# Kernel tuning notes

Hardware: AMD Instinct MI355X
Metric: run time of the kernel (lower is better)

## Reference

```python
import jax, jax.numpy as jnp
import numpy as np

NUM_HEADS = 4
GN_GROUPS = 32
EPS = 1e-5


def setup_inputs() -> dict:
    key = jax.random.key(0)
    ks = jax.random.split(key, 6)
    B, C, H, W = 4, 256, 64, 64
    return {
        "x": jax.random.normal(ks[0], (B, C, H, W), dtype=jnp.float32),
        "gn_w": jnp.ones((C,), dtype=jnp.float32),
        "gn_b": jnp.zeros((C,), dtype=jnp.float32),
        "qkv_w": jax.random.normal(ks[1], (3 * C, C), dtype=jnp.float32) * 0.05,
        "qkv_b": jax.random.normal(ks[2], (3 * C,), dtype=jnp.float32) * 0.02,
        "proj_w": jax.random.normal(ks[3], (C, C), dtype=jnp.float32) * 0.05,
        "proj_b": jax.random.normal(ks[4], (C,), dtype=jnp.float32) * 0.02,
    }


def reference(x, gn_w, gn_b, qkv_w, qkv_b, proj_w, proj_b):
    b, c, h, w = x.shape
    L = h * w
    xf = x.reshape(b, c, L)

    # GroupNorm32: normalize over (channels_per_group, length) in float32
    xg = xf.reshape(b, GN_GROUPS, (c // GN_GROUPS) * L).astype(jnp.float32)
    mean = xg.mean(axis=-1, keepdims=True)
    var = xg.var(axis=-1, keepdims=True)
    xn = ((xg - mean) * jax.lax.rsqrt(var + EPS)).reshape(b, c, L).astype(x.dtype)
    xn = xn * gn_w[:, None] + gn_b[:, None]

    # 1x1 Conv1d == channel matmul: [3C, C] @ [b, C, L]
    qkv = jnp.einsum('oc,bcl->bol', qkv_w, xn) + qkv_b[:, None]

    # QKVAttentionLegacy
    ch = c // NUM_HEADS
    qkv_h = qkv.reshape(b * NUM_HEADS, 3 * ch, L)
    q, k, v = qkv_h[:, :ch], qkv_h[:, ch:2 * ch], qkv_h[:, 2 * ch:]
    scale = 1.0 / np.sqrt(np.sqrt(ch)).astype(np.float32)
    weight = jnp.einsum('bct,bcs->bts', q * scale, k * scale)  # [b*H, L, L]
    weight = jax.nn.softmax(weight.astype(jnp.float32), axis=-1).astype(qkv.dtype)
    a = jnp.einsum('bts,bcs->bct', weight, v).reshape(b, c, L)

    h_out = jnp.einsum('oc,bcl->bol', proj_w, a) + proj_b[:, None]
    return (xf + h_out).reshape(b, c, h, w)
```

## Files before the change

### kernel.cpp

```cpp
#include <hip/hip_runtime.h>
#include <math.h>

#define L 4096
#define C 256

typedef __attribute__((ext_vector_type(8))) short bf16x8;
typedef __attribute__((ext_vector_type(4))) short s16x4;
typedef __attribute__((ext_vector_type(4))) float f32x4;
typedef __attribute__((ext_vector_type(2))) unsigned int u32x2;
typedef __attribute__((ext_vector_type(4))) unsigned int u32x4;

#define MFMA16(a, b, c) __builtin_amdgcn_mfma_f32_16x16x32_bf16(a, b, c, 0, 0, 0)

static __device__ __forceinline__ short f2bf(float f) {
  union { float f; unsigned u; } x{f};
  unsigned r = (x.u + 0x7fffu + ((x.u >> 16) & 1u)) >> 16;
  return (short)r;
}
static __device__ __forceinline__ unsigned pack2(float a, float b) {
  return (unsigned)(unsigned short)f2bf(a) | ((unsigned)(unsigned short)f2bf(b) << 16);
}
static __device__ __forceinline__ unsigned ppack(float a, float b) {
  union { float f; unsigned u; } xa{a}, xb{b};
  return __builtin_amdgcn_perm(xb.u, xa.u, 0x07060302u);
}
static __device__ __forceinline__ void gload_lds16(const void* g, void* l) {
  __builtin_amdgcn_global_load_lds(
      (const __attribute__((address_space(1))) unsigned int*)g,
      (__attribute__((address_space(3))) unsigned int*)l, 16, 0, 0);
}

__global__ __launch_bounds__(256) void prep(const float* __restrict__ x,
    float* __restrict__ gnp, const float* __restrict__ wa,
    const float* __restrict__ wb, short* __restrict__ da,
    short* __restrict__ db) {
  int blk = blockIdx.x;
  int tid = threadIdx.x;
  if (blk < 512) {
    int bg = blk >> 2, q = blk & 3;
    const f32x4* xp = (const f32x4*)(x + (size_t)bg * 32768 + (size_t)q * 8192);
    float s = 0.f, ss = 0.f;
    #pragma unroll
    for (int i = 0; i < 8; ++i) {
      f32x4 v = xp[i * 256 + tid];
      s  += v[0] + v[1] + v[2] + v[3];
      ss += v[0]*v[0] + v[1]*v[1] + v[2]*v[2] + v[3]*v[3];
    }
    __shared__ float rs[256], rss[256];
    rs[tid] = s; rss[tid] = ss;
    __syncthreads();
    for (int off = 128; off > 0; off >>= 1) {
      if (tid < off) { rs[tid] += rs[tid + off]; rss[tid] += rss[tid + off]; }
      __syncthreads();
    }
    if (tid == 0) {
      gnp[(size_t)blk * 2]     = rs[0];
      gnp[(size_t)blk * 2 + 1] = rss[0];
    }
  } else {
    int i = (blk - 512) * 256 + tid;
    if (i < 768 * C) da[i] = f2bf(wa[i]);
    else db[i - 768 * C] = f2bf(wb[i - 768 * C]);
  }
}

__global__ __launch_bounds__(256) void gn_apply(const float* __restrict__ x,
    const float* __restrict__ gw, const float* __restrict__ gb,
    const float* __restrict__ gnp, short* __restrict__ xnT) {
  int bg = blockIdx.y;
  int b = bg >> 5, g = bg & 31;
  int tid = threadIdx.x;
  const float* xg = x + (size_t)bg * 32768;

  float s  = gnp[(size_t)(bg*4)*2]   + gnp[(size_t)(bg*4+1)*2] +
             gnp[(size_t)(bg*4+2)*2] + gnp[(size_t)(bg*4+3)*2];
  float ss = gnp[(size_t)(bg*4)*2+1]   + gnp[(size_t)(bg*4+1)*2+1] +
             gnp[(size_t)(bg*4+2)*2+1] + gnp[(size_t)(bg*4+3)*2+1];
  float mean = s * (1.f / 32768.f);
  float var  = ss * (1.f / 32768.f) - mean * mean;
  float rstd = rsqrtf(var + 1e-5f);

  float scl[8], sft[8];
  #pragma unroll
  for (int c = 0; c < 8; ++c) {
    float wv = gw[g * 8 + c], bv = gb[g * 8 + c];
    scl[c] = rstd * wv;
    sft[c] = bv - mean * rstd * wv;
  }

  short* outb = xnT + (size_t)b * L * C + g * 8;
  int lb = blockIdx.x * 1024 + tid * 4;
  f32x4 v[8];
  #pragma unroll
  for (int c = 0; c < 8; ++c)
    v[c] = *(const f32x4*)(xg + (size_t)c * L + lb);
  #pragma unroll
  for (int j = 0; j < 4; ++j) {
    u32x4 ov;
    #pragma unroll
    for (int cp = 0; cp < 4; ++cp)
      ov[cp] = pack2(v[2*cp][j]   * scl[2*cp]   + sft[2*cp],
                     v[2*cp+1][j] * scl[2*cp+1] + sft[2*cp+1]);
    *(u32x4*)(outb + (size_t)(lb + j) * C) = ov;
  }
}

__global__ __launch_bounds__(256) void qkv_mfma(const short* __restrict__ wq,
    const float* __restrict__ bias, const short* __restrict__ xnT,
    short* __restrict__ qT, short* __restrict__ kT, short* __restrict__ vB) {
  int tid = threadIdx.x;
  int wid = tid >> 6, lane = tid & 63, g = lane >> 4, lr = lane & 15;
  int oy = blockIdx.y;
  int o0 = oy * 64;
  int b  = blockIdx.z;
  int head = oy / 3, kind = oy % 3;
  int bh = b * 4 + head;
  int lw = blockIdx.x * 128 + wid * 32;
  const short* xb = xnT + (size_t)b * L * C;

  f32x4 acc[4][2];
  #pragma unroll
  for (int m = 0; m < 4; ++m)
    #pragma unroll
    for (int nt = 0; nt < 2; ++nt) acc[m][nt] = (f32x4)0.f;

  #pragma unroll 2
  for (int k0 = 0; k0 < C; k0 += 32) {
    bf16x8 af[4], bfr[2];
    #pragma unroll
    for (int m = 0; m < 4; ++m)
      af[m] = *(const bf16x8*)(wq + (size_t)(o0 + m * 16 + lr) * C + k0 + g * 8);
    #pragma unroll
    for (int nt = 0; nt < 2; ++nt)
      bfr[nt] = *(const bf16x8*)(xb + (size_t)(lw + nt * 16 + lr) * C + k0 + g * 8);
    #pragma unroll
    for (int m = 0; m < 4; ++m)
      #pragma unroll
      for (int nt = 0; nt < 2; ++nt)
        acc[m][nt] = MFMA16(af[m], bfr[nt], acc[m][nt]);
  }

  float sc = (kind == 0) ? 0.51014930f : (kind == 1) ? 0.35355339f : 1.0f;
  if (kind == 2) {
    #pragma unroll
    for (int m = 0; m < 4; ++m)
      #pragma unroll
      for (int nt = 0; nt < 2; ++nt)
        #pragma unroll
        for (int r = 0; r < 4; ++r) {
          int o = m * 16 + g * 4 + r;
          vB[((size_t)bh * 64 + o) * L + lw + nt * 16 + lr] =
              f2bf(acc[m][nt][r] + bias[o0 + o]);
        }
  } else {
    short* dst = (kind == 0 ? qT : kT);
    #pragma unroll
    for (int m = 0; m < 4; ++m)
      #pragma unroll
      for (int nt = 0; nt < 2; ++nt) {
        s16x4 pk;
        #pragma unroll
        for (int r = 0; r < 4; ++r)
          pk[r] = f2bf((acc[m][nt][r] + bias[o0 + m * 16 + g * 4 + r]) * sc);
        *(s16x4*)(dst + ((size_t)bh * L + lw + nt * 16 + lr) * 64 + m * 16 + g * 4) = pk;
      }
  }
}

__global__ __launch_bounds__(512) void attn_mfma(
    const short* __restrict__ qT, const short* __restrict__ kT,
    const short* __restrict__ vB, short* __restrict__ amatT) {
  int orig = blockIdx.x;
  int bid = (orig & 7) * 64 + (orig >> 3);
  int bh = bid >> 5, qb = bid & 31;
  int b = bh >> 2, h = bh & 3;
  int tid = threadIdx.x;
  int wid = tid >> 6, lane = tid & 63;
  int g = lane >> 4, lr = lane & 15;
  int tw = qb * 128 + wid * 16;
  int lx7 = lr & 7;
  int pswA = ((lr & 3) << 4) | ((lr >> 2) << 2);

  const short* qTh = qT + (size_t)bh * L * 64;
  const short* kTh = kT + (size_t)bh * L * 64;
  const short* vh  = vB + (size_t)bh * 64 * L;

  __shared__ short Kt[4][64 * 64];
  __shared__ short Vt[4][64 * 64];
  __shared__ short plds[8][16][64];

  bf16x8 qf[2];
  #pragma unroll
  for (int ks = 0; ks < 2; ++ks)
    qf[ks] = *(const bf16x8*)(qTh + (size_t)(tw + lr) * 64 + ks * 32 + g * 8);

  bf16x8 ones;
  #pragma unroll
  for (int i = 0; i < 8; ++i) ones[i] = (short)0x3F80;

  f32x4 acc[4], acc_l;
  #pragma unroll
  for (int cm = 0; cm < 4; ++cm) acc[cm] = (f32x4)0.f;
  acc_l = (f32x4)0.f;

  size_t koff, voff;
  int ldsc;
  {
    int r = tid >> 3, c16 = tid & 7;
    int cs = c16 ^ (r & 7);
    koff = (size_t)r * 64 + cs * 8;
    voff = (size_t)r * L + cs * 8;
    ldsc = wid * 512;
  }

  gload_lds16(kTh + koff, &Kt[0][ldsc]);
  gload_lds16(vh + voff, &Vt[0][ldsc]);
  gload_lds16(kTh + koff + (size_t)64 * 64, &Kt[1][ldsc]);
  gload_lds16(vh + voff + 64, &Vt[1][ldsc]);

  int sl = 0;
  #pragma unroll 1
  for (int s = 0; s < 32; ++s) {
    if (s < 31) {
      int nb = sl ^ 2;
      size_t t0 = (size_t)(2 * s + 2) * 64, t1 = (size_t)(2 * s + 3) * 64;
      gload_lds16(kTh + koff + t0 * 64, &Kt[nb][ldsc]);
      gload_lds16(vh + voff + t0, &Vt[nb][ldsc]);
      gload_lds16(kTh + koff + t1 * 64, &Kt[nb + 1][ldsc]);
      gload_lds16(vh + voff + t1, &Vt[nb + 1][ldsc]);
      asm volatile("s_waitcnt vmcnt(4)" ::: "memory");
    } else {
      asm volatile("s_waitcnt vmcnt(0)" ::: "memory");
    }
    __builtin_amdgcn_sched_barrier(0);
    __builtin_amdgcn_s_barrier();

    const short* Ka = &Kt[sl][0];     const short* Va = &Vt[sl][0];
    const short* Kb = &Kt[sl + 1][0]; const short* Vb = &Vt[sl + 1][0];

    f32x4 st0[4], st1[4];
    __builtin_amdgcn_s_setprio(1);
    #pragma unroll
    for (int sm = 0; sm < 4; ++sm) {
      int row = sm * 16 + lr;
      bf16x8 kf0 = *(const bf16x8*)&Ka[row * 64 + (g ^ lx7) * 8];
      bf16x8 kf1 = *(const bf16x8*)&Ka[row * 64 + ((4 + g) ^ lx7) * 8];
      f32x4 cc = (f32x4)0.f;
      cc = MFMA16(kf0, qf[0], cc);
      cc = MFMA16(kf1, qf[1], cc);
      st0[sm] = cc;
    }
    __builtin_amdgcn_s_setprio(0);
    #pragma unroll
    for (int sm = 0; sm < 4; ++sm) {
      int row = sm * 16 + lr;
      bf16x8 kf0 = *(const bf16x8*)&Kb[row * 64 + (g ^ lx7) * 8];
      bf16x8 kf1 = *(const bf16x8*)&Kb[row * 64 + ((4 + g) ^ lx7) * 8];
      f32x4 cc = (f32x4)0.f;
      cc = MFMA16(kf0, qf[0], cc);
      cc = MFMA16(kf1, qf[1], cc);
      st1[sm] = cc;
      u32x2 w;
      w[0] = ppack(__builtin_amdgcn_exp2f(st0[sm][0]),
                   __builtin_amdgcn_exp2f(st0[sm][1]));
      w[1] = ppack(__builtin_amdgcn_exp2f(st0[sm][2]),
                   __builtin_amdgcn_exp2f(st0[sm][3]));
      *(u32x2*)&plds[wid][lr][(sm * 16 + g * 4) ^ pswA] = w;
    }
    bf16x8 pf0[2];
    #pragma unroll
    for (int ks = 0; ks < 2; ++ks) {
      s16x4 pa = *(const s16x4*)&plds[wid][lr][(ks * 32 + g * 8) ^ pswA];
      s16x4 pb = *(const s16x4*)&plds[wid][lr][(ks * 32 + g * 8 + 4) ^ pswA];
      pf0[ks] = __builtin_shufflevector(pa, pb, 0, 1, 2, 3, 4, 5, 6, 7);
    }
    acc_l = MFMA16(ones, pf0[0], acc_l);
    acc_l = MFMA16(ones, pf0[1], acc_l);
    #pragma unroll
    for (int cm = 0; cm < 4; ++cm) {
      int row = cm * 16 + lr;
      bf16x8 vf0 = *(const bf16x8*)&Va[row * 64 + (g ^ lx7) * 8];
      bf16x8 vf1 = *(const bf16x8*)&Va[row * 64 + ((4 + g) ^ lx7) * 8];
      acc[cm] = MFMA16(vf0, pf0[0], acc[cm]);
      acc[cm] = MFMA16(vf1, pf0[1], acc[cm]);
      u32x2 w;
      w[0] = ppack(__builtin_amdgcn_exp2f(st1[cm][0]),
                   __builtin_amdgcn_exp2f(st1[cm][1]));
      w[1] = ppack(__builtin_amdgcn_exp2f(st1[cm][2]),
                   __builtin_amdgcn_exp2f(st1[cm][3]));
      *(u32x2*)&plds[wid][lr][(cm * 16 + g * 4) ^ pswA] = w;
    }
    bf16x8 pf1[2];
    #pragma unroll
    for (int ks = 0; ks < 2; ++ks) {
      s16x4 pa = *(const s16x4*)&plds[wid][lr][(ks * 32 + g * 8) ^ pswA];
      s16x4 pb = *(const s16x4*)&plds[wid][lr][(ks * 32 + g * 8 + 4) ^ pswA];
      pf1[ks] = __builtin_shufflevector(pa, pb, 0, 1, 2, 3, 4, 5, 6, 7);
    }
    __builtin_amdgcn_s_setprio(1);
    acc_l = MFMA16(ones, pf1[0], acc_l);
    acc_l = MFMA16(ones, pf1[1], acc_l);
    #pragma unroll
    for (int cm = 0; cm < 4; ++cm) {
      int row = cm * 16 + lr;
      bf16x8 vf0 = *(const bf16x8*)&Vb[row * 64 + (g ^ lx7) * 8];
      bf16x8 vf1 = *(const bf16x8*)&Vb[row * 64 + ((4 + g) ^ lx7) * 8];
      acc[cm] = MFMA16(vf0, pf1[0], acc[cm]);
      acc[cm] = MFMA16(vf1, pf1[1], acc[cm]);
    }
    __builtin_amdgcn_s_setprio(0);
    __builtin_amdgcn_s_barrier();
    sl ^= 2;
  }

  float inv = 1.f / acc_l[0];
  #pragma unroll
  for (int cm = 0; cm < 4; ++cm) {
    s16x4 pk;
    #pragma unroll
    for (int r = 0; r < 4; ++r) pk[r] = f2bf(acc[cm][r] * inv);
    *(s16x4*)(amatT + ((size_t)b * L + tw + lr) * C + h * 64 + cm * 16 + g * 4) = pk;
  }
}

__global__ __launch_bounds__(256) void proj_mfma(const short* __restrict__ pw,
    const float* __restrict__ bias, const short* __restrict__ amatT,
    const float* __restrict__ xres, float* __restrict__ out) {
  int tid = threadIdx.x;
  int wid = tid >> 6, lane = tid & 63, g = lane >> 4, lr = lane & 15;
  int o0 = blockIdx.y * 64;
  int b  = blockIdx.z;
  int lw = blockIdx.x * 128 + wid * 32;
  const short* ab = amatT + (size_t)b * L * C;

  f32x4 acc[4][2];
  #pragma unroll
  for (int m = 0; m < 4; ++m)
    #pragma unroll
    for (int nt = 0; nt < 2; ++nt) acc[m][nt] = (f32x4)0.f;

  #pragma unroll 2
  for (int k0 = 0; k0 < C; k0 += 32) {
    bf16x8 af[4], bfr[2];
    #pragma unroll
    for (int m = 0; m < 4; ++m)
      af[m] = *(const bf16x8*)(pw + (size_t)(o0 + m * 16 + lr) * C + k0 + g * 8);
    #pragma unroll
    for (int nt = 0; nt < 2; ++nt)
      bfr[nt] = *(const bf16x8*)(ab + (size_t)(lw + nt * 16 + lr) * C + k0 + g * 8);
    #pragma unroll
    for (int m = 0; m < 4; ++m)
      #pragma unroll
      for (int nt = 0; nt < 2; ++nt)
        acc[m][nt] = MFMA16(af[m], bfr[nt], acc[m][nt]);
  }

  #pragma unroll
  for (int m = 0; m < 4; ++m)
    #pragma unroll
    for (int nt = 0; nt < 2; ++nt)
      #pragma unroll
      for (int r = 0; r < 4; ++r) {
        int o = o0 + m * 16 + g * 4 + r;
        size_t idx = ((size_t)b * C + o) * L + lw + nt * 16 + lr;
        out[idx] = acc[m][nt][r] + bias[o] + xres[idx];
      }
}

extern "C" void kernel_launch(void* const* d_in, const int* in_sizes, int n_in,
                              void* d_out, int out_size, void* d_ws, size_t ws_size,
                              hipStream_t stream) {
  const float* x      = (const float*)d_in[0];
  const float* gn_w   = (const float*)d_in[1];
  const float* gn_b   = (const float*)d_in[2];
  const float* qkv_w  = (const float*)d_in[3];
  const float* qkv_b  = (const float*)d_in[4];
  const float* proj_w = (const float*)d_in[5];
  const float* proj_b = (const float*)d_in[6];
  float* out = (float*)d_out;

  short* xnT   = (short*)d_ws;
  short* qT    = xnT   + (size_t)4 * L * C;
  short* kT    = qT    + (size_t)16 * L * 64;
  short* vB    = kT    + (size_t)16 * L * 64;
  short* amatT = vB    + (size_t)16 * L * 64;
  short* wqbf  = amatT + (size_t)4 * L * C;
  short* pwbf  = wqbf  + (size_t)768 * C;
  float* gnp   = (float*)(pwbf + (size_t)C * C);

  prep<<<1536, 256, 0, stream>>>(x, gnp, qkv_w, proj_w, wqbf, pwbf);
  gn_apply<<<dim3(4, 128), 256, 0, stream>>>(x, gn_w, gn_b, gnp, xnT);
  qkv_mfma<<<dim3(32, 12, 4), 256, 0, stream>>>(wqbf, qkv_b, xnT, qT, kT, vB);
  attn_mfma<<<512, 512, 0, stream>>>(qT, kT, vB, amatT);
  proj_mfma<<<dim3(32, 4, 4), 256, 0, stream>>>(pwbf, proj_b, amatT, x, out);
}
```

Measured before the change: 152.1 us.

## Process two 16-row query tiles per wave in attention to reuse K/V fragments

Each wave in the attention kernel now handles 32 query rows, as two 16-row tiles, instead of 16. The block therefore covers 256 queries and the grid halves from 512 to 256 blocks. Each K/V fragment read from LDS and each staged K/V tile is reused across twice as many MFMAs, cutting LDS and global traffic per unit of work. The cost is roughly double the accumulator and score registers, a larger P scratch buffer in LDS, and only 256 blocks on a 256-CU part, which lowers occupancy and may hurt latency hiding.

```diff
diff --git a/kernel.cpp b/kernel.cpp
--- a/kernel.cpp
+++ b/kernel.cpp
@@ -171,13 +171,13 @@
     const short* __restrict__ qT, const short* __restrict__ kT,
     const short* __restrict__ vB, short* __restrict__ amatT) {
   int orig = blockIdx.x;
-  int bid = (orig & 7) * 64 + (orig >> 3);
-  int bh = bid >> 5, qb = bid & 31;
+  int bid = (orig & 7) * 32 + (orig >> 3);
+  int bh = bid >> 4, qb = bid & 15;
   int b = bh >> 2, h = bh & 3;
   int tid = threadIdx.x;
   int wid = tid >> 6, lane = tid & 63;
   int g = lane >> 4, lr = lane & 15;
-  int tw = qb * 128 + wid * 16;
+  int tw = qb * 256 + wid * 32;
   int lx7 = lr & 7;
   int pswA = ((lr & 3) << 4) | ((lr >> 2) << 2);
 
@@ -187,21 +187,26 @@
 
   __shared__ short Kt[4][64 * 64];
   __shared__ short Vt[4][64 * 64];
-  __shared__ short plds[8][16][64];
-
-  bf16x8 qf[2];
-  #pragma unroll
-  for (int ks = 0; ks < 2; ++ks)
-    qf[ks] = *(const bf16x8*)(qTh + (size_t)(tw + lr) * 64 + ks * 32 + g * 8);
+  __shared__ short plds[8][32][64];
+
+  bf16x8 qf[2][2];
+  #pragma unroll
+  for (int nt = 0; nt < 2; ++nt)
+    #pragma unroll
+    for (int ks = 0; ks < 2; ++ks)
+      qf[nt][ks] = *(const bf16x8*)(qTh + (size_t)(tw + nt * 16 + lr) * 64 +
+                                    ks * 32 + g * 8);
 
   bf16x8 ones;
   #pragma unroll
   for (int i = 0; i < 8; ++i) ones[i] = (short)0x3F80;
 
-  f32x4 acc[4], acc_l;
-  #pragma unroll
-  for (int cm = 0; cm < 4; ++cm) acc[cm] = (f32x4)0.f;
-  acc_l = (f32x4)0.f;
+  f32x4 acc[4][2], acc_l[2];
+  #pragma unroll
+  for (int cm = 0; cm < 4; ++cm)
+    #pragma unroll
+    for (int nt = 0; nt < 2; ++nt) acc[cm][nt] = (f32x4)0.f;
+  acc_l[0] = (f32x4)0.f; acc_l[1] = (f32x4)0.f;
 
   size_t koff, voff;
   int ldsc;
@@ -238,17 +243,20 @@
     const short* Ka = &Kt[sl][0];     const short* Va = &Vt[sl][0];
     const short* Kb = &Kt[sl + 1][0]; const short* Vb = &Vt[sl + 1][0];
 
-    f32x4 st0[4], st1[4];
+    f32x4 st0[4][2], st1[4][2];
     __builtin_amdgcn_s_setprio(1);
     #pragma unroll
     for (int sm = 0; sm < 4; ++sm) {
       int row = sm * 16 + lr;
       bf16x8 kf0 = *(const bf16x8*)&Ka[row * 64 + (g ^ lx7) * 8];
       bf16x8 kf1 = *(const bf16x8*)&Ka[row * 64 + ((4 + g) ^ lx7) * 8];
-      f32x4 cc = (f32x4)0.f;
-      cc = MFMA16(kf0, qf[0], cc);
-      cc = MFMA16(kf1, qf[1], cc);
-      st0[sm] = cc;
+      #pragma unroll
+      for (int nt = 0; nt < 2; ++nt) {
+        f32x4 cc = (f32x4)0.f;
+        cc = MFMA16(kf0, qf[nt][0], cc);
+        cc = MFMA16(kf1, qf[nt][1], cc);
+        st0[sm][nt] = cc;
+      }
     }
     __builtin_amdgcn_s_setprio(0);
     #pragma unroll
@@ -256,70 +264,93 @@
       int row = sm * 16 + lr;
       bf16x8 kf0 = *(const bf16x8*)&Kb[row * 64 + (g ^ lx7) * 8];
       bf16x8 kf1 = *(const bf16x8*)&Kb[row * 64 + ((4 + g) ^ lx7) * 8];
-      f32x4 cc = (f32x4)0.f;
-      cc = MFMA16(kf0, qf[0], cc);
-      cc = MFMA16(kf1, qf[1], cc);
-      st1[sm] = cc;
-      u32x2 w;
-      w[0] = ppack(__builtin_amdgcn_exp2f(st0[sm][0]),
-                   __builtin_amdgcn_exp2f(st0[sm][1]));
-      w[1] = ppack(__builtin_amdgcn_exp2f(st0[sm][2]),
-                   __builtin_amdgcn_exp2f(st0[sm][3]));
-      *(u32x2*)&plds[wid][lr][(sm * 16 + g * 4) ^ pswA] = w;
-    }
-    bf16x8 pf0[2];
-    #pragma unroll
-    for (int ks = 0; ks < 2; ++ks) {
-      s16x4 pa = *(const s16x4*)&plds[wid][lr][(ks * 32 + g * 8) ^ pswA];
-      s16x4 pb = *(const s16x4*)&plds[wid][lr][(ks * 32 + g * 8 + 4) ^ pswA];
-      pf0[ks] = __builtin_shufflevector(pa, pb, 0, 1, 2, 3, 4, 5, 6, 7);
-    }
-    acc_l = MFMA16(ones, pf0[0], acc_l);
-    acc_l = MFMA16(ones, pf0[1], acc_l);
+      #pragma unroll
+      for (int nt = 0; nt < 2; ++nt) {
+        f32x4 cc = (f32x4)0.f;
+        cc = MFMA16(kf0, qf[nt][0], cc);
+        cc = MFMA16(kf1, qf[nt][1], cc);
+        st1[sm][nt] = cc;
+        u32x2 w;
+        w[0] = ppack(__builtin_amdgcn_exp2f(st0[sm][nt][0]),
+                     __builtin_amdgcn_exp2f(st0[sm][nt][1]));
+        w[1] = ppack(__builtin_amdgcn_exp2f(st0[sm][nt][2]),
+                     __builtin_amdgcn_exp2f(st0[sm][nt][3]));
+        *(u32x2*)&plds[wid][nt * 16 + lr][(sm * 16 + g * 4) ^ pswA] = w;
+      }
+    }
+    bf16x8 pf0[2][2];
+    #pragma unroll
+    for (int nt = 0; nt < 2; ++nt)
+      #pragma unroll
+      for (int ks = 0; ks < 2; ++ks) {
+        s16x4 pa = *(const s16x4*)&plds[wid][nt * 16 + lr][(ks * 32 + g * 8) ^ pswA];
+        s16x4 pb = *(const s16x4*)&plds[wid][nt * 16 + lr][(ks * 32 + g * 8 + 4) ^ pswA];
+        pf0[nt][ks] = __builtin_shufflevector(pa, pb, 0, 1, 2, 3, 4, 5, 6, 7);
+      }
+    #pragma unroll
+    for (int nt = 0; nt < 2; ++nt) {
+      acc_l[nt] = MFMA16(ones, pf0[nt][0], acc_l[nt]);
+      acc_l[nt] = MFMA16(ones, pf0[nt][1], acc_l[nt]);
+    }
     #pragma unroll
     for (int cm = 0; cm < 4; ++cm) {
       int row = cm * 16 + lr;
       bf16x8 vf0 = *(const bf16x8*)&Va[row * 64 + (g ^ lx7) * 8];
       bf16x8 vf1 = *(const bf16x8*)&Va[row * 64 + ((4 + g) ^ lx7) * 8];
-      acc[cm] = MFMA16(vf0, pf0[0], acc[cm]);
-      acc[cm] = MFMA16(vf1, pf0[1], acc[cm]);
-      u32x2 w;
-      w[0] = ppack(__builtin_amdgcn_exp2f(st1[cm][0]),
-                   __builtin_amdgcn_exp2f(st1[cm][1]));
-      w[1] = ppack(__builtin_amdgcn_exp2f(st1[cm][2]),
-                   __builtin_amdgcn_exp2f(st1[cm][3]));
-      *(u32x2*)&plds[wid][lr][(cm * 16 + g * 4) ^ pswA] = w;
-    }
-    bf16x8 pf1[2];
-    #pragma unroll
-    for (int ks = 0; ks < 2; ++ks) {
-      s16x4 pa = *(const s16x4*)&plds[wid][lr][(ks * 32 + g * 8) ^ pswA];
-      s16x4 pb = *(const s16x4*)&plds[wid][lr][(ks * 32 + g * 8 + 4) ^ pswA];
-      pf1[ks] = __builtin_shufflevector(pa, pb, 0, 1, 2, 3, 4, 5, 6, 7);
-    }
+      #pragma unroll
+      for (int nt = 0; nt < 2; ++nt) {
+        acc[cm][nt] = MFMA16(vf0, pf0[nt][0], acc[cm][nt]);
+        acc[cm][nt] = MFMA16(vf1, pf0[nt][1], acc[cm][nt]);
+        u32x2 w;
+        w[0] = ppack(__builtin_amdgcn_exp2f(st1[cm][nt][0]),
+                     __builtin_amdgcn_exp2f(st1[cm][nt][1]));
+        w[1] = ppack(__builtin_amdgcn_exp2f(st1[cm][nt][2]),
+                     __builtin_amdgcn_exp2f(st1[cm][nt][3]));
+        *(u32x2*)&plds[wid][nt * 16 + lr][(cm * 16 + g * 4) ^ pswA] = w;
+      }
+    }
+    bf16x8 pf1[2][2];
+    #pragma unroll
+    for (int nt = 0; nt < 2; ++nt)
+      #pragma unroll
+      for (int ks = 0; ks < 2; ++ks) {
+        s16x4 pa = *(const s16x4*)&plds[wid][nt * 16 + lr][(ks * 32 + g * 8) ^ pswA];
+        s16x4 pb = *(const s16x4*)&plds[wid][nt * 16 + lr][(ks * 32 + g * 8 + 4) ^ pswA];
+        pf1[nt][ks] = __builtin_shufflevector(pa, pb, 0, 1, 2, 3, 4, 5, 6, 7);
+      }
     __builtin_amdgcn_s_setprio(1);
-    acc_l = MFMA16(ones, pf1[0], acc_l);
-    acc_l = MFMA16(ones, pf1[1], acc_l);
+    #pragma unroll
+    for (int nt = 0; nt < 2; ++nt) {
+      acc_l[nt] = MFMA16(ones, pf1[nt][0], acc_l[nt]);
+      acc_l[nt] = MFMA16(ones, pf1[nt][1], acc_l[nt]);
+    }
     #pragma unroll
     for (int cm = 0; cm < 4; ++cm) {
       int row = cm * 16 + lr;
       bf16x8 vf0 = *(const bf16x8*)&Vb[row * 64 + (g ^ lx7) * 8];
       bf16x8 vf1 = *(const bf16x8*)&Vb[row * 64 + ((4 + g) ^ lx7) * 8];
-      acc[cm] = MFMA16(vf0, pf1[0], acc[cm]);
-      acc[cm] = MFMA16(vf1, pf1[1], acc[cm]);
+      #pragma unroll
+      for (int nt = 0; nt < 2; ++nt) {
+        acc[cm][nt] = MFMA16(vf0, pf1[nt][0], acc[cm][nt]);
+        acc[cm][nt] = MFMA16(vf1, pf1[nt][1], acc[cm][nt]);
+      }
     }
     __builtin_amdgcn_s_setprio(0);
     __builtin_amdgcn_s_barrier();
     sl ^= 2;
   }
 
-  float inv = 1.f / acc_l[0];
-  #pragma unroll
-  for (int cm = 0; cm < 4; ++cm) {
-    s16x4 pk;
-    #pragma unroll
-    for (int r = 0; r < 4; ++r) pk[r] = f2bf(acc[cm][r] * inv);
-    *(s16x4*)(amatT + ((size_t)b * L + tw + lr) * C + h * 64 + cm * 16 + g * 4) = pk;
+  #pragma unroll
+  for (int nt = 0; nt < 2; ++nt) {
+    float inv = 1.f / acc_l[nt][0];
+    #pragma unroll
+    for (int cm = 0; cm < 4; ++cm) {
+      s16x4 pk;
+      #pragma unroll
+      for (int r = 0; r < 4; ++r) pk[r] = f2bf(acc[cm][nt][r] * inv);
+      *(s16x4*)(amatT + ((size_t)b * L + tw + nt * 16 + lr) * C + h * 64 +
+                cm * 16 + g * 4) = pk;
+    }
   }
 }
 
@@ -391,6 +422,6 @@
   prep<<<1536, 256, 0, stream>>>(x, gnp, qkv_w, proj_w, wqbf, pwbf);
   gn_apply<<<dim3(4, 128), 256, 0, stream>>>(x, gn_w, gn_b, gnp, xnT);
   qkv_mfma<<<dim3(32, 12, 4), 256, 0, stream>>>(wqbf, qkv_b, xnT, qT, kT, vB);
-  attn_mfma<<<512, 512, 0, stream>>>(qT, kT, vB, amatT);
+  attn_mfma<<<256, 512, 0, stream>>>(qT, kT, vB, amatT);
   proj_mfma<<<dim3(32, 4, 4), 256, 0, stream>>>(pwbf, proj_b, amatT, x, out);
 }
```

Result: faster. 148.9 us (-2.1%).

## Switch attention to 32x32x16 MFMA with register shuffles for P

Applied to the files above, without the earlier changes.

The attention kernel moves from 16x16x32 to 32x32x16 bf16 MFMA tiles, so each wave handles 32 query rows and a block covers 256 queries, which halves the grid to 256 blocks. The P matrix is now rebuilt in registers with cross-half lane shuffles instead of going through an LDS staging buffer. The row sum is computed with scalar adds plus one shuffle, replacing the extra ones-matrix MFMAs. This removes LDS traffic and MFMA overhead per K/V byte loaded, but it raises register pressure and leaves fewer blocks than the 256 CUs can hide latency with.

```diff
diff --git a/kernel.cpp b/kernel.cpp
--- a/kernel.cpp
+++ b/kernel.cpp
@@ -7,10 +7,12 @@
 typedef __attribute__((ext_vector_type(8))) short bf16x8;
 typedef __attribute__((ext_vector_type(4))) short s16x4;
 typedef __attribute__((ext_vector_type(4))) float f32x4;
+typedef __attribute__((ext_vector_type(16))) float f32x16;
 typedef __attribute__((ext_vector_type(2))) unsigned int u32x2;
 typedef __attribute__((ext_vector_type(4))) unsigned int u32x4;
 
 #define MFMA16(a, b, c) __builtin_amdgcn_mfma_f32_16x16x32_bf16(a, b, c, 0, 0, 0)
+#define MFMA32(a, b, c) __builtin_amdgcn_mfma_f32_32x32x16_bf16(a, b, c, 0, 0, 0)
 
 static __device__ __forceinline__ short f2bf(float f) {
   union { float f; unsigned u; } x{f};
@@ -23,6 +25,12 @@
 static __device__ __forceinline__ unsigned ppack(float a, float b) {
   union { float f; unsigned u; } xa{a}, xb{b};
   return __builtin_amdgcn_perm(xb.u, xa.u, 0x07060302u);
+}
+static __device__ __forceinline__ bf16x8 mk8(unsigned a, unsigned b,
+                                             unsigned c, unsigned d) {
+  union { u32x4 u; bf16x8 v; } x;
+  x.u[0] = a; x.u[1] = b; x.u[2] = c; x.u[3] = d;
+  return x.v;
 }
 static __device__ __forceinline__ void gload_lds16(const void* g, void* l) {
   __builtin_amdgcn_global_load_lds(
@@ -171,15 +179,13 @@
     const short* __restrict__ qT, const short* __restrict__ kT,
     const short* __restrict__ vB, short* __restrict__ amatT) {
   int orig = blockIdx.x;
-  int bid = (orig & 7) * 64 + (orig >> 3);
-  int bh = bid >> 5, qb = bid & 31;
+  int bid = (orig & 7) * 32 + (orig >> 3);
+  int bh = bid >> 4, qb = bid & 15;
   int b = bh >> 2, h = bh & 3;
   int tid = threadIdx.x;
   int wid = tid >> 6, lane = tid & 63;
-  int g = lane >> 4, lr = lane & 15;
-  int tw = qb * 128 + wid * 16;
-  int lx7 = lr & 7;
-  int pswA = ((lr & 3) << 4) | ((lr >> 2) << 2);
+  int l31 = lane & 31, hi = lane >> 5;
+  int tw = qb * 256 + wid * 32;
 
   const short* qTh = qT + (size_t)bh * L * 64;
   const short* kTh = kT + (size_t)bh * L * 64;
@@ -187,21 +193,14 @@
 
   __shared__ short Kt[4][64 * 64];
   __shared__ short Vt[4][64 * 64];
-  __shared__ short plds[8][16][64];
-
-  bf16x8 qf[2];
-  #pragma unroll
-  for (int ks = 0; ks < 2; ++ks)
-    qf[ks] = *(const bf16x8*)(qTh + (size_t)(tw + lr) * 64 + ks * 32 + g * 8);
-
-  bf16x8 ones;
-  #pragma unroll
-  for (int i = 0; i < 8; ++i) ones[i] = (short)0x3F80;
-
-  f32x4 acc[4], acc_l;
-  #pragma unroll
-  for (int cm = 0; cm < 4; ++cm) acc[cm] = (f32x4)0.f;
-  acc_l = (f32x4)0.f;
+
+  bf16x8 qf[4];
+  #pragma unroll
+  for (int kd = 0; kd < 4; ++kd)
+    qf[kd] = *(const bf16x8*)(qTh + (size_t)(tw + l31) * 64 + kd * 16 + hi * 8);
+
+  f32x16 accO0 = (f32x16)0.f, accO1 = (f32x16)0.f;
+  float ls0 = 0.f, ls1 = 0.f;
 
   size_t koff, voff;
   int ldsc;
@@ -212,6 +211,28 @@
     voff = (size_t)r * L + cs * 8;
     ldsc = wid * 512;
   }
+
+  auto KF = [&](const short* base, int row, int c16) {
+    return *(const bf16x8*)&base[row * 64 + ((c16 ^ (row & 7)) << 3)];
+  };
+
+  auto SMF = [&](const f32x16& st, bf16x8& pf0, bf16x8& pf1) {
+    unsigned pw[8], sw[8];
+    #pragma unroll
+    for (int q = 0; q < 8; ++q) {
+      float e0 = __builtin_amdgcn_exp2f(st[2 * q]);
+      float e1 = __builtin_amdgcn_exp2f(st[2 * q + 1]);
+      ls0 += e0; ls1 += e1;
+      pw[q] = ppack(e0, e1);
+    }
+    #pragma unroll
+    for (int q = 0; q < 8; ++q)
+      sw[q] = (unsigned)__shfl_xor((int)pw[q], 32);
+    pf0 = mk8(hi ? sw[2] : pw[0], hi ? sw[3] : pw[1],
+              hi ? pw[2] : sw[0], hi ? pw[3] : sw[1]);
+    pf1 = mk8(hi ? sw[6] : pw[4], hi ? sw[7] : pw[5],
+              hi ? pw[6] : sw[4], hi ? pw[7] : sw[5]);
+  };
 
   gload_lds16(kTh + koff, &Kt[0][ldsc]);
   gload_lds16(vh + voff, &Vt[0][ldsc]);
@@ -238,88 +259,60 @@
     const short* Ka = &Kt[sl][0];     const short* Va = &Vt[sl][0];
     const short* Kb = &Kt[sl + 1][0]; const short* Vb = &Vt[sl + 1][0];
 
-    f32x4 st0[4], st1[4];
+    f32x16 sA0 = (f32x16)0.f, sA1 = (f32x16)0.f;
     __builtin_amdgcn_s_setprio(1);
     #pragma unroll
-    for (int sm = 0; sm < 4; ++sm) {
-      int row = sm * 16 + lr;
-      bf16x8 kf0 = *(const bf16x8*)&Ka[row * 64 + (g ^ lx7) * 8];
-      bf16x8 kf1 = *(const bf16x8*)&Ka[row * 64 + ((4 + g) ^ lx7) * 8];
-      f32x4 cc = (f32x4)0.f;
-      cc = MFMA16(kf0, qf[0], cc);
-      cc = MFMA16(kf1, qf[1], cc);
-      st0[sm] = cc;
+    for (int kd = 0; kd < 4; ++kd) {
+      sA0 = MFMA32(KF(Ka, l31, hi + 2 * kd), qf[kd], sA0);
+      sA1 = MFMA32(KF(Ka, 32 + l31, hi + 2 * kd), qf[kd], sA1);
     }
     __builtin_amdgcn_s_setprio(0);
-    #pragma unroll
-    for (int sm = 0; sm < 4; ++sm) {
-      int row = sm * 16 + lr;
-      bf16x8 kf0 = *(const bf16x8*)&Kb[row * 64 + (g ^ lx7) * 8];
-      bf16x8 kf1 = *(const bf16x8*)&Kb[row * 64 + ((4 + g) ^ lx7) * 8];
-      f32x4 cc = (f32x4)0.f;
-      cc = MFMA16(kf0, qf[0], cc);
-      cc = MFMA16(kf1, qf[1], cc);
-      st1[sm] = cc;
-      u32x2 w;
-      w[0] = ppack(__builtin_amdgcn_exp2f(st0[sm][0]),
-                   __builtin_amdgcn_exp2f(st0[sm][1]));
-      w[1] = ppack(__builtin_amdgcn_exp2f(st0[sm][2]),
-                   __builtin_amdgcn_exp2f(st0[sm][3]));
-      *(u32x2*)&plds[wid][lr][(sm * 16 + g * 4) ^ pswA] = w;
-    }
-    bf16x8 pf0[2];
-    #pragma unroll
-    for (int ks = 0; ks < 2; ++ks) {
-      s16x4 pa = *(const s16x4*)&plds[wid][lr][(ks * 32 + g * 8) ^ pswA];
-      s16x4 pb = *(const s16x4*)&plds[wid][lr][(ks * 32 + g * 8 + 4) ^ pswA];
-      pf0[ks] = __builtin_shufflevector(pa, pb, 0, 1, 2, 3, 4, 5, 6, 7);
-    }
-    acc_l = MFMA16(ones, pf0[0], acc_l);
-    acc_l = MFMA16(ones, pf0[1], acc_l);
-    #pragma unroll
-    for (int cm = 0; cm < 4; ++cm) {
-      int row = cm * 16 + lr;
-      bf16x8 vf0 = *(const bf16x8*)&Va[row * 64 + (g ^ lx7) * 8];
-      bf16x8 vf1 = *(const bf16x8*)&Va[row * 64 + ((4 + g) ^ lx7) * 8];
-      acc[cm] = MFMA16(vf0, pf0[0], acc[cm]);
-      acc[cm] = MFMA16(vf1, pf0[1], acc[cm]);
-      u32x2 w;
-      w[0] = ppack(__builtin_amdgcn_exp2f(st1[cm][0]),
-                   __builtin_amdgcn_exp2f(st1[cm][1]));
-      w[1] = ppack(__builtin_amdgcn_exp2f(st1[cm][2]),
-                   __builtin_amdgcn_exp2f(st1[cm][3]));
-      *(u32x2*)&plds[wid][lr][(cm * 16 + g * 4) ^ pswA] = w;
-    }
-    bf16x8 pf1[2];
-    #pragma unroll
-    for (int ks = 0; ks < 2; ++ks) {
-      s16x4 pa = *(const s16x4*)&plds[wid][lr][(ks * 32 + g * 8) ^ pswA];
-      s16x4 pb = *(const s16x4*)&plds[wid][lr][(ks * 32 + g * 8 + 4) ^ pswA];
-      pf1[ks] = __builtin_shufflevector(pa, pb, 0, 1, 2, 3, 4, 5, 6, 7);
-    }
+
+    f32x16 sB0 = (f32x16)0.f, sB1 = (f32x16)0.f;
+    #pragma unroll
+    for (int kd = 0; kd < 4; ++kd) {
+      sB0 = MFMA32(KF(Kb, l31, hi + 2 * kd), qf[kd], sB0);
+      sB1 = MFMA32(KF(Kb, 32 + l31, hi + 2 * kd), qf[kd], sB1);
+    }
+    bf16x8 pA[4];
+    SMF(sA0, pA[0], pA[1]);
+    SMF(sA1, pA[2], pA[3]);
+
+    bf16x8 pB[4];
+    SMF(sB0, pB[0], pB[1]);
+    SMF(sB1, pB[2], pB[3]);
+    #pragma unroll
+    for (int m = 0; m < 4; ++m) {
+      accO0 = MFMA32(KF(Va, l31, hi + 2 * m), pA[m], accO0);
+      accO1 = MFMA32(KF(Va, 32 + l31, hi + 2 * m), pA[m], accO1);
+    }
+
     __builtin_amdgcn_s_setprio(1);
-    acc_l = MFMA16(ones, pf1[0], acc_l);
-    acc_l = MFMA16(ones, pf1[1], acc_l);
-    #pragma unroll
-    for (int cm = 0; cm < 4; ++cm) {
-      int row = cm * 16 + lr;
-      bf16x8 vf0 = *(const bf16x8*)&Vb[row * 64 + (g ^ lx7) * 8];
-      bf16x8 vf1 = *(const bf16x8*)&Vb[row * 64 + ((4 + g) ^ lx7) * 8];
-      acc[cm] = MFMA16(vf0, pf1[0], acc[cm]);
-      acc[cm] = MFMA16(vf1, pf1[1], acc[cm]);
+    #pragma unroll
+    for (int m = 0; m < 4; ++m) {
+      accO0 = MFMA32(KF(Vb, l31, hi + 2 * m), pB[m], accO0);
+      accO1 = MFMA32(KF(Vb, 32 + l31, hi + 2 * m), pB[m], accO1);
     }
     __builtin_amdgcn_s_setprio(0);
     __builtin_amdgcn_s_barrier();
     sl ^= 2;
   }
 
-  float inv = 1.f / acc_l[0];
-  #pragma unroll
-  for (int cm = 0; cm < 4; ++cm) {
-    s16x4 pk;
-    #pragma unroll
-    for (int r = 0; r < 4; ++r) pk[r] = f2bf(acc[cm][r] * inv);
-    *(s16x4*)(amatT + ((size_t)b * L + tw + lr) * C + h * 64 + cm * 16 + g * 4) = pk;
+  float lst = ls0 + ls1;
+  lst += __shfl_xor(lst, 32);
+  float inv = 1.f / lst;
+
+  #pragma unroll
+  for (int dt = 0; dt < 2; ++dt) {
+    #pragma unroll
+    for (int q = 0; q < 4; ++q) {
+      s16x4 pk;
+      #pragma unroll
+      for (int r = 0; r < 4; ++r)
+        pk[r] = f2bf((dt ? accO1[4 * q + r] : accO0[4 * q + r]) * inv);
+      int d = h * 64 + dt * 32 + q * 8 + 4 * hi;
+      *(s16x4*)(amatT + ((size_t)b * L + tw + l31) * C + d) = pk;
+    }
   }
 }
 
@@ -391,6 +384,6 @@
   prep<<<1536, 256, 0, stream>>>(x, gnp, qkv_w, proj_w, wqbf, pwbf);
   gn_apply<<<dim3(4, 128), 256, 0, stream>>>(x, gn_w, gn_b, gnp, xnT);
   qkv_mfma<<<dim3(32, 12, 4), 256, 0, stream>>>(wqbf, qkv_b, xnT, qT, kT, vB);
-  attn_mfma<<<512, 512, 0, stream>>>(qT, kT, vB, amatT);
+  attn_mfma<<<256, 512, 0, stream>>>(qT, kT, vB, amatT);
   proj_mfma<<<dim3(32, 4, 4), 256, 0, stream>>>(pwbf, proj_b, amatT, x, out);
 }
```

Result: slower. 168.7 us (+10.9%).
